# Kernel tuning notes

Measured on AMD Instinct MI355X. Metric: run time of the kernel, lower is better.

Reference implementation:

```python
import jax, jax.numpy as jnp
import numpy as np

EPS = 1e-5
NB, NP, NA, NROT = 16, 1024, 12, 60
C0, C1 = 64, 128
CIN, CFEAT, COUT = 256, 512, 256


def _bn(x, g, b):
    # training-mode BatchNorm1d: stats over batch (+ spatial) dims, channel dim 1
    axes = (0,) if x.ndim == 2 else (0, 2)
    m = x.mean(axis=axes, keepdims=True)
    v = x.var(axis=axes, keepdims=True)
    sh = [1] * x.ndim; sh[1] = -1
    return (x - m) * jax.lax.rsqrt(v + EPS) * g.reshape(sh) + b.reshape(sh)


def _hat(v):  # (n,3) -> (n,3,3) skew-symmetric
    z = jnp.zeros_like(v[:, 0])
    return jnp.stack([z, -v[:, 2], v[:, 1],
                      v[:, 2], z, -v[:, 0],
                      -v[:, 1], v[:, 0], z], axis=-1).reshape(-1, 3, 3)


def _exp_so3(v):  # Rodrigues formula, (n,3) -> (n,3,3)
    theta = jnp.linalg.norm(v, axis=-1, keepdims=True)  # (n,1)
    k = v / jnp.where(theta < 1e-8, 1.0, theta)
    K = _hat(k)
    s = jnp.sin(theta)[..., None]
    c = (1.0 - jnp.cos(theta))[..., None]
    I = jnp.eye(3, dtype=v.dtype)
    return I + s * K + c * (K @ K)


def _pointnet(xyz, feats, W, b, g, bb):
    # PointnetSO3Conv: concat xyz (expanded over anchors) with feats, 1x1 conv, max over points
    nb, _, npts, na = feats.shape
    x = jnp.concatenate([jnp.broadcast_to(xyz[:, :, :, None], (nb, 3, npts, na)), feats], axis=1)
    y = jnp.einsum('oc,bcpa->bopa', W, x) + b[None, :, None, None]
    y = y.max(axis=2)  # max over points -> (nb, o, na)
    return jax.nn.relu(_bn(y, g, bb))


def setup_inputs() -> dict:
    key = jax.random.key(0)
    ks = iter(jax.random.split(key, 64))
    def nrm(shape, s=0.1):
        return jax.random.normal(next(ks), shape, dtype=jnp.float32) * s
    d = {
        'xyz0': nrm((NB, 3, NP), 1.0),
        'feats0': nrm((NB, C0, NP, NA), 1.0),
        'xyz1': nrm((NB, 3, NP), 1.0),
        'feats1': nrm((NB, C1, NP, NA), 1.0),
        'trace_idx': jax.random.randint(next(ks), (NA, NROT), 0, NA),
        'anchors': nrm((NROT, 3, 3), 1.0),
        'pn0_W': nrm((C0, C0 + 3)), 'pn0_b': nrm((C0,)), 'pn0_g': jnp.ones((C0,), jnp.float32), 'pn0_bb': jnp.zeros((C0,), jnp.float32),
        'pn1_W': nrm((C1, C1 + 3)), 'pn1_b': nrm((C1,)), 'pn1_g': jnp.ones((C1,), jnp.float32), 'pn1_bb': jnp.zeros((C1,), jnp.float32),
        'lin_W': nrm((CIN, C0 + C1)), 'lin_b': nrm((CIN,)), 'lin_g': jnp.ones((CIN,), jnp.float32), 'lin_bb': jnp.zeros((CIN,), jnp.float32),
        'feat_W': nrm((CFEAT, CIN * NA)), 'feat_b': nrm((CFEAT,)), 'feat_g': jnp.ones((CFEAT,), jnp.float32), 'feat_bb': jnp.zeros((CFEAT,), jnp.float32),
        'att_W1': nrm((128, CFEAT)), 'att_b1': nrm((128,)), 'att_g': jnp.ones((128,), jnp.float32), 'att_bb': jnp.zeros((128,), jnp.float32),
        'att_W2': nrm((1, 128)), 'att_b2': nrm((1,)),
        'reg_W1': nrm((128, CFEAT)), 'reg_b1': nrm((128,)), 'reg_g': jnp.ones((128,), jnp.float32), 'reg_bb': jnp.zeros((128,), jnp.float32),
        'reg_W2': nrm((7, 128)), 'reg_b2': nrm((7,)),
        'out_W1': nrm((CFEAT, CFEAT)), 'out_b1': nrm((CFEAT,)), 'out_g': jnp.ones((CFEAT,), jnp.float32), 'out_bb': jnp.zeros((CFEAT,), jnp.float32),
        'out_W2': nrm((COUT, CFEAT)), 'out_b2': nrm((COUT,)),
    }
    return d


def reference(xyz0, feats0, xyz1, feats1, trace_idx, anchors,
              pn0_W, pn0_b, pn0_g, pn0_bb, pn1_W, pn1_b, pn1_g, pn1_bb,
              lin_W, lin_b, lin_g, lin_bb, feat_W, feat_b, feat_g, feat_bb,
              att_W1, att_b1, att_g, att_bb, att_W2, att_b2,
              reg_W1, reg_b1, reg_g, reg_bb, reg_W2, reg_b2,
              out_W1, out_b1, out_g, out_bb, out_W2, out_b2):
    nb = feats0.shape[0]
    # _pooling: per-level pointnet + BN + relu, concat, pn_linear + pn_bn
    p0 = _pointnet(xyz0, feats0, pn0_W, pn0_b, pn0_g, pn0_bb)
    p1 = _pointnet(xyz1, feats1, pn1_W, pn1_b, pn1_g, pn1_bb)
    x = jnp.concatenate([p0, p1], axis=1)                                   # (nb, 192, na)
    x = _bn(jnp.einsum('oc,bca->boa', lin_W, x) + lin_b[None, :, None], lin_g, lin_bb)  # (nb,256,na)
    # gather trace_idx_ori and flatten channel x anchor dims
    x = x[:, :, trace_idx].reshape(nb, CIN * NA, NROT)                      # (nb,3072,60)
    xf = jax.nn.relu(_bn(jnp.einsum('oc,bca->boa', feat_W, x) + feat_b[None, :, None], feat_g, feat_bb))  # (nb,512,60)
    h = jax.nn.relu(_bn(jnp.einsum('oc,bca->boa', reg_W1, xf) + reg_b1[None, :, None], reg_g, reg_bb))
    residual = (jnp.einsum('oc,bca->boa', reg_W2, h) + reg_b2[None, :, None]).transpose(0, 2, 1)  # (nb,60,7)
    res_D = residual[:, :, :3] / jnp.linalg.norm(residual[:, :, :3], axis=-1, keepdims=True)
    res_N = (jax.nn.sigmoid(residual[:, :, 3]) - 0.5) * jnp.pi / 5
    res_V = res_D * res_N[..., None]
    res_R = _exp_so3(res_V.reshape(-1, 3)).reshape(nb, NROT, 3, 3)
    res_T = residual[:, :, 4:]
    pred_R = jnp.einsum('tij,btjk->btik', anchors, res_R)
    # attention head + softmax over 60 rotations
    a = jax.nn.relu(_bn(jnp.einsum('oc,bca->boa', att_W1, xf) + att_b1[None, :, None], att_g, att_bb))
    logits = (jnp.einsum('oc,bca->boa', att_W2, a) + att_b2[None, :, None])[:, 0]   # (nb,60)
    x_attn = jax.nn.softmax(logits, axis=-1)
    # max-pool over rotations + out MLP
    xm = xf.max(axis=-1)                                                    # (nb,512)
    o = jax.nn.relu(_bn(xm @ out_W1.T + out_b1, out_g, out_bb))
    x_out = o @ out_W2.T + out_b2
    return (x_out, x_attn, pred_R, res_T)
```

## Files before the change

kernel.cpp:

```cpp
#include <hip/hip_runtime.h>
#include <math.h>

#define NBATCH 16
#define NPTS   1024
#define NANG   12
#define NROTS  60
#define EPSV   1e-5f

#define WB0_OFF   0
#define WB1_OFF   3072
#define PART0_OFF 13312
#define PART1_OFF 799744
#define XF_OFF    13312
#define XM_OFF    504832
#define OACT_OFF  513024
#define XCAT_OFF  2372608
#define XLIN_OFF  2409472
#define XG_OFF    2458624
#define BRP_OFF   2458624
#define HACT_OFF  4424704
#define AACT_OFF  4547584
#define FRAW_OFF  5407744
#define FEATW_OFF 6882304
#define XP0_OFF   8455168
#define XP1_OFF   14746624

#define OUT_XOUT 0
#define OUT_ATTN 4096
#define OUT_PRED 5056
#define OUT_REST 13696

typedef short  bf16x8 __attribute__((ext_vector_type(8)));
typedef float  f32x4  __attribute__((ext_vector_type(4)));

__device__ __forceinline__ unsigned short f2bf_rne(float x){
  unsigned int u = __float_as_uint(x);
  u += 0x7FFFu + ((u >> 16) & 1u);
  return (unsigned short)(u >> 16);
}
__device__ __forceinline__ float bf2f(unsigned short h){
  return __uint_as_float(((unsigned int)h) << 16);
}

__device__ __forceinline__ bf16x8 pack8(const float* f){
  union { unsigned int u[4]; bf16x8 v; } r;
  #pragma unroll
  for (int i = 0; i < 4; i++)
    r.u[i] = __builtin_amdgcn_perm(__float_as_uint(f[2*i+1]),
                                   __float_as_uint(f[2*i]), 0x07060302u);
  return r.v;
}

__device__ __forceinline__ void stage16(const unsigned short* g, unsigned short* l){
  __builtin_amdgcn_global_load_lds((const __attribute__((address_space(1))) void*)g,
                                   (__attribute__((address_space(3))) void*)l, 16, 0, 0);
}

template<int NT>
__device__ __forceinline__ void block_stats(float v, float& m, float& var, float* sbuf){
  constexpr int NW = NT / 64;
  float s = v, s2 = v * v;
  #pragma unroll
  for (int off = 32; off; off >>= 1){
    s  += __shfl_xor(s,  off, 64);
    s2 += __shfl_xor(s2, off, 64);
  }
  const int w = threadIdx.x >> 6;
  if ((threadIdx.x & 63) == 0){ sbuf[w] = s; sbuf[NW + w] = s2; }
  __syncthreads();
  float ts = 0.f, ts2 = 0.f;
  #pragma unroll
  for (int i = 0; i < NW; i++){ ts += sbuf[i]; ts2 += sbuf[NW + i]; }
  m = ts / (float)NT;
  var = ts2 / (float)NT - m * m;
}

#define TB0 6248
#define TB1 7784
template<int C>
__device__ __forceinline__ void prep_wb_body(int idx, const float* __restrict__ W,
                                             unsigned short* __restrict__ Wb){
  constexpr int KPAD = C + 32;
  if (idx >= C * KPAD) return;
  const int o = idx / KPAD, k = idx % KPAD;
  float v = 0.f;
  if (k < C)          v = W[(size_t)o * (C + 3) + 3 + k];
  else if (k < C + 3) v = W[(size_t)o * (C + 3) + (k - C)];
  Wb[idx] = f2bf_rne(v);
}

__global__ __launch_bounds__(256) void prep_all(
    const float* __restrict__ W0, const float* __restrict__ W1,
    const float* __restrict__ FW,
    const float* __restrict__ feats0, const float* __restrict__ feats1,
    unsigned short* __restrict__ wb0, unsigned short* __restrict__ wb1,
    unsigned short* __restrict__ fw2,
    unsigned short* __restrict__ xp0, unsigned short* __restrict__ xp1){
  __shared__ unsigned short tr[32][258];
  const int blk = blockIdx.x;
  if (blk < 24){
    prep_wb_body<64>(blk * 256 + threadIdx.x, W0, wb0);
    return;
  }
  if (blk < 104){
    prep_wb_body<128>((blk - 24) * 256 + threadIdx.x, W1, wb1);
    return;
  }
  if (blk < TB0){
    const int idx = (blk - 104) * 256 + threadIdx.x;
    const int o = idx / 3072, k = idx % 3072;
    const float x = FW[idx];
    const unsigned short hi = f2bf_rne(x);
    const unsigned short lo = f2bf_rne(x - bf2f(hi));
    fw2[(size_t)o * 6144 + k] = hi;
    fw2[(size_t)o * 6144 + 3072 + k] = lo;
    return;
  }
  const float* src; unsigned short* dst;
  if (blk < TB1){
    const int tb = blk - TB0;
    const int nt = tb % 48, kt = tb / 48;
    src = feats0 + (size_t)kt * 32 * 12288 + nt * 256;
    dst = xp0 + ((size_t)kt * 12288 + nt * 256) * 32;
  } else {
    const int tb = blk - TB1;
    const int nt = tb % 48, kt = tb / 48;
    src = feats1 + (size_t)kt * 32 * 12288 + nt * 256;
    dst = xp1 + ((size_t)kt * 12288 + nt * 256) * 32;
  }
  const int t = threadIdx.x;
  #pragma unroll
  for (int q = 0; q < 8; q++){
    const int idx = q * 256 + t;
    const int rr = idx >> 6, c4 = (idx & 63) << 2;
    const float4 v = *(const float4*)(src + (size_t)rr * 12288 + c4);
    tr[rr][c4 + 0] = (unsigned short)(__float_as_uint(v.x) >> 16);
    tr[rr][c4 + 1] = (unsigned short)(__float_as_uint(v.y) >> 16);
    tr[rr][c4 + 2] = (unsigned short)(__float_as_uint(v.z) >> 16);
    tr[rr][c4 + 3] = (unsigned short)(__float_as_uint(v.w) >> 16);
  }
  __syncthreads();
  union { unsigned short s[32]; bf16x8 v8[4]; } ob;
  #pragma unroll
  for (int j = 0; j < 32; j++) ob.s[j] = tr[j][t];
  unsigned short* dp = dst + (size_t)t * 32;
  #pragma unroll
  for (int q = 0; q < 4; q++)
    *(bf16x8*)(dp + q * 8) = ob.v8[q];
}

#define SROW 196
template<int C>
__device__ __forceinline__ void pn_body(
    int nchunk, int b,
    const float* __restrict__ xyz, const unsigned short* __restrict__ Xp,
    const unsigned short* __restrict__ Wb, float* __restrict__ part,
    float* yb ){
  constexpr int KPAD = C + 32;
  constexpr int NFK  = C / 32;
  constexpr int MTH  = C / 32;
  const int tid  = threadIdx.x;
  const int lane = tid & 63, w = tid >> 6;
  const int wo = w >> 2, wn = w & 3;
  const int g = lane >> 4, l16 = lane & 15;
  const int o_off = wo * (C / 2);
  const int nbase = nchunk * 192;

  int nn[3], pp[3];
  #pragma unroll
  for (int t = 0; t < 3; t++){
    nn[t] = wn * 48 + t * 16 + l16;
    pp[t] = (nbase + nn[t]) / 12;
  }

  f32x4 acc[MTH][3];
  #pragma unroll
  for (int m = 0; m < MTH; m++)
    #pragma unroll
    for (int t = 0; t < 3; t++)
      acc[m][t] = (f32x4){0.f, 0.f, 0.f, 0.f};

  const unsigned short* xbase = Xp + (size_t)b * NFK * 12288 * 32 + g * 8;
  bf16x8 Bf[NFK][3];
  #pragma unroll
  for (int ks = 0; ks < NFK; ks++)
    #pragma unroll
    for (int t = 0; t < 3; t++)
      Bf[ks][t] = *(const bf16x8*)(xbase + ((size_t)ks * 12288 + nbase + nn[t]) * 32);

  #pragma unroll
  for (int ks = 0; ks < NFK; ks++){
    const int kb = ks * 32;
    #pragma unroll
    for (int m = 0; m < MTH; m++){
      const bf16x8 Af = *(const bf16x8*)(Wb + (size_t)(o_off + m * 16 + l16) * KPAD + kb + g * 8);
      #pragma unroll
      for (int t = 0; t < 3; t++)
        acc[m][t] = __builtin_amdgcn_mfma_f32_16x16x32_bf16(Af, Bf[ks][t], acc[m][t], 0, 0, 0);
    }
  }

  {
    const int kb = C;
    bf16x8 Bf2[3];
    #pragma unroll
    for (int t = 0; t < 3; t++){
      float f[8];
      #pragma unroll
      for (int j = 0; j < 8; j++) f[j] = 0.f;
      if (g == 0){
        #pragma unroll
        for (int j = 0; j < 3; j++)
          f[j] = xyz[(size_t)(b * 3 + j) * NPTS + pp[t]];
      }
      Bf2[t] = pack8(f);
    }
    #pragma unroll
    for (int m = 0; m < MTH; m++){
      const bf16x8 Af = *(const bf16x8*)(Wb + (size_t)(o_off + m * 16 + l16) * KPAD + kb + g * 8);
      #pragma unroll
      for (int t = 0; t < 3; t++)
        acc[m][t] = __builtin_amdgcn_mfma_f32_16x16x32_bf16(Af, Bf2[t], acc[m][t], 0, 0, 0);
    }
  }

  float* myb = yb + wo * (16 * SROW);
  #pragma unroll
  for (int m = 0; m < MTH; m++){
    __syncthreads();
    #pragma unroll
    for (int t = 0; t < 3; t++)
      #pragma unroll
      for (int r = 0; r < 4; r++)
        myb[(g * 4 + r) * SROW + nn[t]] = acc[m][t][r];
    __syncthreads();
    const int lt = tid & 255;
    if (lt < 192){
      const int o_l = lt / 12, a = lt % 12;
      float mx = -3.4e38f;
      #pragma unroll
      for (int pl = 0; pl < 16; pl++)
        mx = fmaxf(mx, myb[o_l * SROW + pl * 12 + a]);
      part[((size_t)(b * 64 + nchunk) * C + o_off + m * 16 + o_l) * 12 + a] = mx;
    }
  }
}

__global__ __launch_bounds__(512, 4) void pn_both(
    const float* __restrict__ xyz0, const unsigned short* __restrict__ xp0,
    const unsigned short* __restrict__ wb0, float* __restrict__ part0,
    const float* __restrict__ xyz1, const unsigned short* __restrict__ xp1,
    const unsigned short* __restrict__ wb1, float* __restrict__ part1){
  __shared__ float yb[2 * 16 * SROW];
  const int lin   = blockIdx.x + 64 * (blockIdx.y + 16 * blockIdx.z);
  const int which = lin & 1;
  const int rest  = lin >> 1;
  const int nchunk = rest & 63, b = rest >> 6;
  if (which == 0) pn_body<64> (nchunk, b, xyz0, xp0, wb0, part0, yb);
  else            pn_body<128>(nchunk, b, xyz1, xp1, wb1, part1, yb);
}

__global__ void pn_reduce_bn(const float* __restrict__ part0, const float* __restrict__ part1,
    const float* __restrict__ b0, const float* __restrict__ g0, const float* __restrict__ bb0,
    const float* __restrict__ b1, const float* __restrict__ g1, const float* __restrict__ bb1,
    float* __restrict__ xcat){
  const int ch = blockIdx.x, t = threadIdx.x;
  const int b = t / 12, a = t % 12;
  const float* part; const float *bias, *g, *bb; int o, Cl;
  if (ch < 64){ part = part0; bias = b0; g = g0; bb = bb0; o = ch;      Cl = 64;  }
  else        { part = part1; bias = b1; g = g1; bb = bb1; o = ch - 64; Cl = 128; }
  const float* pp = part + ((size_t)(b * 64) * Cl + o) * 12 + a;
  const size_t kstride = (size_t)Cl * 12;
  float v = pp[0];
  for (int k = 1; k < 64; k++) v = fmaxf(v, pp[(size_t)k * kstride]);
  v += bias[o];
  __shared__ float sbuf[8];
  float m, var;
  block_stats<192>(v, m, var, sbuf);
  float xn = (v - m) * rsqrtf(var + EPSV) * g[o] + bb[o];
  xcat[((size_t)b * 192 + ch) * 12 + a] = fmaxf(xn, 0.f);
}

__global__ void lin_bn(const float* __restrict__ xcat, const float* __restrict__ W,
    const float* __restrict__ bias, const float* __restrict__ g, const float* __restrict__ bb,
    float* __restrict__ xlin){
  const int o = blockIdx.x, t = threadIdx.x;
  const int b = t / 12, a = t % 12;
  const float* xr = xcat + (size_t)b * 2304 + a;
  const float* wr = W + (size_t)o * 192;
  float v = bias[o];
  for (int c = 0; c < 192; c++) v = fmaf(wr[c], xr[(size_t)c * 12], v);
  __shared__ float sbuf[8];
  float m, var;
  block_stats<192>(v, m, var, sbuf);
  xlin[((size_t)b * 256 + o) * 12 + a] = (v - m) * rsqrtf(var + EPSV) * g[o] + bb[o];
}

__global__ void prep_xg(const float* __restrict__ xlin, const int* __restrict__ trace,
                        unsigned short* __restrict__ Xg){
  const int n = blockIdx.x;
  const int b = n / 60, r = n % 60;
  unsigned short* row = Xg + (size_t)n * 6144;
  __shared__ int ta[12];
  if (threadIdx.x < 12) ta[threadIdx.x] = trace[threadIdx.x * 60 + r];
  __syncthreads();
  for (int i = threadIdx.x; i < 3072; i += 256){
    const int c = i / 12, a = i % 12;
    const float x = xlin[((size_t)b * 256 + c) * 12 + ta[a]];
    const unsigned short hi = f2bf_rne(x);
    const unsigned short lo = f2bf_rne(x - bf2f(hi));
    row[i] = hi;
    row[3072 + i] = lo;
  }
}

__global__ __launch_bounds__(256) void feat_mfma(
    const unsigned short* __restrict__ Wb2, const unsigned short* __restrict__ Xg,
    float* __restrict__ fraw){
  const int nblk = blockIdx.x, mblk = blockIdx.y, seg = blockIdx.z;
  const int tid = threadIdx.x;
  const int lane = tid & 63, wave = tid >> 6;
  const int g = lane >> 4, l16 = lane & 15;
  const int kA = (seg == 1) ? 3072 : 0;
  const int kB = (seg == 2) ? 3072 : 0;
  const int sw = l16 & 7;
  const int wm = wave >> 1, wn = wave & 1;

  __shared__ unsigned short As[2][64 * 64];
  __shared__ unsigned short Bs[2][64 * 64];

  int rowj[2], colj[2], ldsoff[2];
  #pragma unroll
  for (int j = 0; j < 2; j++){
    const int idx = j * 256 + wave * 64 + lane;
    rowj[j]   = idx >> 3;
    colj[j]   = ((idx & 7) ^ (rowj[j] & 7)) * 8;
    ldsoff[j] = (j * 256 + wave * 64) * 8;
  }
  const unsigned short* Agb = Wb2 + (size_t)mblk * 64 * 6144 + kA;
  const unsigned short* Bgb = Xg  + (size_t)nblk * 64 * 6144 + kB;

  f32x4 acc[2][2];
  #pragma unroll
  for (int i = 0; i < 2; i++)
    #pragma unroll
    for (int j = 0; j < 2; j++)
      acc[i][j] = (f32x4){0.f, 0.f, 0.f, 0.f};

  #pragma unroll
  for (int j = 0; j < 2; j++){
    stage16(Agb + (size_t)rowj[j] * 6144 + colj[j], &As[0][ldsoff[j]]);
    stage16(Bgb + (size_t)rowj[j] * 6144 + colj[j], &Bs[0][ldsoff[j]]);
  }
  __syncthreads();

  for (int kc = 0; kc < 3072; kc += 64){
    const int buf = (kc >> 6) & 1;
    if (kc + 64 < 3072){
      const int kn = kc + 64;
      #pragma unroll
      for (int j = 0; j < 2; j++){
        stage16(Agb + (size_t)rowj[j] * 6144 + kn + colj[j], &As[buf ^ 1][ldsoff[j]]);
        stage16(Bgb + (size_t)rowj[j] * 6144 + kn + colj[j], &Bs[buf ^ 1][ldsoff[j]]);
      }
    }
    #pragma unroll
    for (int kc2 = 0; kc2 < 64; kc2 += 32){
      const int c0 = kc2 >> 3;
      bf16x8 af[2], bfr[2];
      #pragma unroll
      for (int i = 0; i < 2; i++)
        af[i]  = *(const bf16x8*)&As[buf][(wm * 32 + i * 16 + l16) * 64 + ((c0 + g) ^ sw) * 8];
      #pragma unroll
      for (int i = 0; i < 2; i++)
        bfr[i] = *(const bf16x8*)&Bs[buf][(wn * 32 + i * 16 + l16) * 64 + ((c0 + g) ^ sw) * 8];
      #pragma unroll
      for (int i = 0; i < 2; i++)
        #pragma unroll
        for (int j = 0; j < 2; j++)
          acc[i][j] = __builtin_amdgcn_mfma_f32_16x16x32_bf16(af[i], bfr[j], acc[i][j], 0, 0, 0);
    }
    __syncthreads();
  }

  float* base = fraw + (size_t)seg * (512 * 960);
  #pragma unroll
  for (int i = 0; i < 2; i++)
    #pragma unroll
    for (int j = 0; j < 2; j++){
      const int n = nblk * 64 + wn * 32 + j * 16 + l16;
      #pragma unroll
      for (int q = 0; q < 4; q++){
        const int m = mblk * 64 + wm * 32 + i * 16 + g * 4 + q;
        base[(size_t)m * 960 + n] = acc[i][j][q];
      }
    }
}

__global__ void feat_bn(const float* __restrict__ fraw, const float* __restrict__ bias,
    const float* __restrict__ g, const float* __restrict__ bb,
    float* __restrict__ xf, float* __restrict__ xm){
  const int o = blockIdx.x, t = threadIdx.x;
  const int b = t / 60, r = t % 60;
  const size_t SS = (size_t)512 * 960;
  const size_t in = (size_t)o * 960 + t;
  float v = fraw[in] + fraw[SS + in] + fraw[2 * SS + in] + bias[o];
  __shared__ float sbuf[32];
  float m, var;
  block_stats<960>(v, m, var, sbuf);
  const float xn = fmaxf((v - m) * rsqrtf(var + EPSV) * g[o] + bb[o], 0.f);
  xf[((size_t)b * 512 + o) * 60 + r] = xn;
  __shared__ float red[960];
  red[t] = xn;
  __syncthreads();
  if (r == 0){
    float mx = red[t];
    for (int k = 1; k < 60; k++) mx = fmaxf(mx, red[t + k]);
    xm[(size_t)b * 512 + o] = mx;
  }
}

__global__ __launch_bounds__(256) void brgemm_oh1(const float* __restrict__ xf,
    const float* __restrict__ Wr, const float* __restrict__ Wa,
    float* __restrict__ brp,
    const float* __restrict__ xm, const float* __restrict__ oW1,
    const float* __restrict__ ob1, const float* __restrict__ og,
    const float* __restrict__ obb, float* __restrict__ o_act){
  const int z = blockIdx.z;
  if (z == 16){
    const int q = blockIdx.y * 4 + blockIdx.x;
    if (q >= 32) return;
    const int t = threadIdx.x;
    const int b = t & 15, j = t >> 4;
    const int oc = q * 16 + j;
    float acc = ob1[oc];
    const float* wr = oW1 + (size_t)oc * 512;
    const float* xr = xm + (size_t)b * 512;
    for (int c = 0; c < 512; c++) acc = fmaf(wr[c], xr[c], acc);
    float s = acc, s2 = acc * acc;
    #pragma unroll
    for (int off = 8; off; off >>= 1){
      s  += __shfl_xor(s,  off, 16);
      s2 += __shfl_xor(s2, off, 16);
    }
    const float m = s * (1.f / 16.f);
    const float var = s2 * (1.f / 16.f) - m * m;
    o_act[(size_t)b * 512 + oc] = fmaxf((acc - m) * rsqrtf(var + EPSV) * og[oc] + obb[oc], 0.f);
    return;
  }
  const int og_ = blockIdx.x, b = blockIdx.y;
  const int br = z >> 3, ks = z & 7;
  const float* W = br ? Wa : Wr;
  const int lane = threadIdx.x & 63, wave = threadIdx.x >> 6;
  const int obase = og_ * 32 + wave * 8;
  const int rr = lane < 60 ? lane : 0;
  const float* xb = xf + ((size_t)b * 512 + ks * 64) * 60 + rr;
  const float* wr = W + (size_t)obase * 512 + ks * 64;

  float acc[8];
  #pragma unroll
  for (int i = 0; i < 8; i++) acc[i] = 0.f;

  float cur[4], nxt[4];
  #pragma unroll
  for (int j = 0; j < 4; j++) cur[j] = xb[(size_t)j * 60];

  for (int c0 = 0; c0 < 64; c0 += 4){
    #pragma unroll
    for (int j = 0; j < 4; j++){
      int cc = c0 + 4 + j; if (cc > 63) cc = 63;
      nxt[j] = xb[(size_t)cc * 60];
    }
    #pragma unroll
    for (int j = 0; j < 4; j++)
      #pragma unroll
      for (int i = 0; i < 8; i++)
        acc[i] = fmaf(wr[(size_t)i * 512 + c0 + j], cur[j], acc[i]);
    #pragma unroll
    for (int j = 0; j < 4; j++) cur[j] = nxt[j];
  }

  if (lane < 60){
    #pragma unroll
    for (int i = 0; i < 8; i++)
      brp[(((size_t)z * NBATCH + b) * 128 + obase + i) * 60 + lane] = acc[i];
  }
}

__global__ void br_bn(const float* __restrict__ brp,
    const float* __restrict__ biasR, const float* __restrict__ gR, const float* __restrict__ bbR,
    const float* __restrict__ biasA, const float* __restrict__ gA, const float* __restrict__ bbA,
    float* __restrict__ hact, float* __restrict__ aact){
  const int o = blockIdx.x, br = blockIdx.y, t = threadIdx.x;
  const int b = t / 60, r = t % 60;
  const float* bias = br ? biasA : biasR;
  const float* g    = br ? gA    : gR;
  const float* bb   = br ? bbA   : bbR;
  float v = bias[o];
  #pragma unroll
  for (int ks = 0; ks < 8; ks++)
    v += brp[((((size_t)br * 8 + ks) * NBATCH + b) * 128 + o) * 60 + r];
  __shared__ float sbuf[32];
  float m, var;
  block_stats<960>(v, m, var, sbuf);
  float* outp = br ? aact : hact;
  outp[((size_t)b * 128 + o) * 60 + r] =
      fmaxf((v - m) * rsqrtf(var + EPSV) * g[o] + bb[o], 0.f);
}

__global__ void heads(
    const float* __restrict__ h, const float* __restrict__ rW2,
    const float* __restrict__ rb2, const float* __restrict__ anchors,
    const float* __restrict__ a, const float* __restrict__ aW2, const float* __restrict__ ab2,
    const float* __restrict__ o_act, const float* __restrict__ oW2,
    const float* __restrict__ ob2, float* __restrict__ out){
  const int b = blockIdx.x, sel = blockIdx.y, t = threadIdx.x;
  if (sel == 0){
    if (t >= 64) return;
    const int r = t < 60 ? t : 59;
    float res[7];
    #pragma unroll
    for (int j = 0; j < 7; j++) res[j] = rb2[j];
    for (int c = 0; c < 128; c++){
      const float hv = h[((size_t)b * 128 + c) * 60 + r];
      #pragma unroll
      for (int j = 0; j < 7; j++) res[j] = fmaf(rW2[j * 128 + c], hv, res[j]);
    }
    if (t >= 60) return;
    const float n = sqrtf(res[0]*res[0] + res[1]*res[1] + res[2]*res[2]);
    const float invn = 1.f / n;
    const float Nv = (1.f / (1.f + expf(-res[3])) - 0.5f) * 3.14159265358979323846f / 5.f;
    const float v0 = res[0]*invn*Nv, v1 = res[1]*invn*Nv, v2 = res[2]*invn*Nv;
    const float th = sqrtf(v0*v0 + v1*v1 + v2*v2);
    const float invt = th < 1e-8f ? 1.f : 1.f / th;
    const float k0 = v0*invt, k1 = v1*invt, k2 = v2*invt;
    const float s = sinf(th), cc = 1.f - cosf(th);
    const float K[9] = {0.f, -k2, k1,  k2, 0.f, -k0,  -k1, k0, 0.f};
    float K2[9];
    #pragma unroll
    for (int ii = 0; ii < 3; ii++)
      #pragma unroll
      for (int jj = 0; jj < 3; jj++)
        K2[ii*3+jj] = K[ii*3+0]*K[0*3+jj] + K[ii*3+1]*K[1*3+jj] + K[ii*3+2]*K[2*3+jj];
    float R[9];
    #pragma unroll
    for (int ii = 0; ii < 3; ii++)
      #pragma unroll
      for (int jj = 0; jj < 3; jj++)
        R[ii*3+jj] = (ii == jj ? 1.f : 0.f) + s * K[ii*3+jj] + cc * K2[ii*3+jj];
    const float* A = anchors + (size_t)t * 9;
    #pragma unroll
    for (int ii = 0; ii < 3; ii++)
      #pragma unroll
      for (int kk = 0; kk < 3; kk++){
        const float pv = A[ii*3+0]*R[0*3+kk] + A[ii*3+1]*R[1*3+kk] + A[ii*3+2]*R[2*3+kk];
        out[OUT_PRED + ((size_t)b * 60 + t) * 9 + ii * 3 + kk] = pv;
      }
    #pragma unroll
    for (int k = 0; k < 3; k++)
      out[OUT_REST + ((size_t)b * 60 + t) * 3 + k] = res[4 + k];
  } else if (sel == 1){
    if (t >= 64) return;
    const int r = t < 60 ? t : 59;
    float acc = ab2[0];
    for (int c = 0; c < 128; c++)
      acc = fmaf(aW2[c], a[((size_t)b * 128 + c) * 60 + r], acc);
    const float l = t < 60 ? acc : -INFINITY;
    float mx = l;
    #pragma unroll
    for (int off = 32; off; off >>= 1) mx = fmaxf(mx, __shfl_xor(mx, off, 64));
    const float e = t < 60 ? expf(l - mx) : 0.f;
    float ssum = e;
    #pragma unroll
    for (int off = 32; off; off >>= 1) ssum += __shfl_xor(ssum, off, 64);
    if (t < 60) out[OUT_ATTN + (size_t)b * 60 + t] = e / ssum;
  } else {
    const float* wr = oW2 + (size_t)t * 512;
    const float* xr = o_act + (size_t)b * 512;
    float acc = ob2[t];
    for (int c = 0; c < 512; c++) acc = fmaf(wr[c], xr[c], acc);
    out[OUT_XOUT + (size_t)b * 256 + t] = acc;
  }
}

extern "C" void kernel_launch(void* const* d_in, const int* in_sizes, int n_in,
                              void* d_out, int out_size, void* d_ws, size_t ws_size,
                              hipStream_t stream){
  const float* xyz0    = (const float*)d_in[0];
  const float* feats0  = (const float*)d_in[1];
  const float* xyz1    = (const float*)d_in[2];
  const float* feats1  = (const float*)d_in[3];
  const int*   trace   = (const int*)  d_in[4];
  const float* anchors = (const float*)d_in[5];
  const float* pn0_W  = (const float*)d_in[6];
  const float* pn0_b  = (const float*)d_in[7];
  const float* pn0_g  = (const float*)d_in[8];
  const float* pn0_bb = (const float*)d_in[9];
  const float* pn1_W  = (const float*)d_in[10];
  const float* pn1_b  = (const float*)d_in[11];
  const float* pn1_g  = (const float*)d_in[12];
  const float* pn1_bb = (const float*)d_in[13];
  const float* lin_W  = (const float*)d_in[14];
  const float* lin_b  = (const float*)d_in[15];
  const float* lin_g  = (const float*)d_in[16];
  const float* lin_bb = (const float*)d_in[17];
  const float* feat_W  = (const float*)d_in[18];
  const float* feat_b  = (const float*)d_in[19];
  const float* feat_g  = (const float*)d_in[20];
  const float* feat_bb = (const float*)d_in[21];
  const float* att_W1 = (const float*)d_in[22];
  const float* att_b1 = (const float*)d_in[23];
  const float* att_g  = (const float*)d_in[24];
  const float* att_bb = (const float*)d_in[25];
  const float* att_W2 = (const float*)d_in[26];
  const float* att_b2 = (const float*)d_in[27];
  const float* reg_W1 = (const float*)d_in[28];
  const float* reg_b1 = (const float*)d_in[29];
  const float* reg_g  = (const float*)d_in[30];
  const float* reg_bb = (const float*)d_in[31];
  const float* reg_W2 = (const float*)d_in[32];
  const float* reg_b2 = (const float*)d_in[33];
  const float* out_W1 = (const float*)d_in[34];
  const float* out_b1 = (const float*)d_in[35];
  const float* out_g  = (const float*)d_in[36];
  const float* out_bb = (const float*)d_in[37];
  const float* out_W2 = (const float*)d_in[38];
  const float* out_b2 = (const float*)d_in[39];

  float* ws  = (float*)d_ws;
  float* out = (float*)d_out;
  unsigned short* wb0 = (unsigned short*)(ws + WB0_OFF);
  unsigned short* wb1 = (unsigned short*)(ws + WB1_OFF);
  unsigned short* fw  = (unsigned short*)(ws + FEATW_OFF);
  unsigned short* xg  = (unsigned short*)(ws + XG_OFF);
  unsigned short* xp0 = (unsigned short*)(ws + XP0_OFF);
  unsigned short* xp1 = (unsigned short*)(ws + XP1_OFF);

  prep_all<<<10856, 256, 0, stream>>>(pn0_W, pn1_W, feat_W, feats0, feats1,
                                      wb0, wb1, fw, xp0, xp1);

  pn_both<<<dim3(64, 16, 2), 512, 0, stream>>>(xyz0, xp0, wb0, ws + PART0_OFF,
                                               xyz1, xp1, wb1, ws + PART1_OFF);

  pn_reduce_bn<<<192, 192, 0, stream>>>(ws + PART0_OFF, ws + PART1_OFF,
      pn0_b, pn0_g, pn0_bb, pn1_b, pn1_g, pn1_bb, ws + XCAT_OFF);

  lin_bn<<<256, 192, 0, stream>>>(ws + XCAT_OFF, lin_W, lin_b, lin_g, lin_bb, ws + XLIN_OFF);

  prep_xg<<<960, 256, 0, stream>>>(ws + XLIN_OFF, trace, xg);

  feat_mfma<<<dim3(15, 8, 3), 256, 0, stream>>>(fw, xg, ws + FRAW_OFF);

  feat_bn<<<512, 960, 0, stream>>>(ws + FRAW_OFF, feat_b, feat_g, feat_bb,
                                   ws + XF_OFF, ws + XM_OFF);

  brgemm_oh1<<<dim3(4, 16, 17), 256, 0, stream>>>(ws + XF_OFF, reg_W1, att_W1, ws + BRP_OFF,
      ws + XM_OFF, out_W1, out_b1, out_g, out_bb, ws + OACT_OFF);

  br_bn<<<dim3(128, 2), 960, 0, stream>>>(ws + BRP_OFF,
      reg_b1, reg_g, reg_bb, att_b1, att_g, att_bb,
      ws + HACT_OFF, ws + AACT_OFF);

  heads<<<dim3(16, 3), 256, 0, stream>>>(ws + HACT_OFF, reg_W2, reg_b2, anchors,
      ws + AACT_OFF, att_W2, att_b2, ws + OACT_OFF, out_W2, out_b2, out);
}
```

Baseline: 466.1 us.

## Split prep and pointnet launches to overlap feats1 transpose with pn0 compute

Prep of the weights and the feats0 transpose now run in their own kernel. A second kernel runs the feats1 transpose, the pn0 pointnet GEMM and the split of the feat weights into hi/lo bf16 together, and pn1 gets a separate launch. The goal is to overlap the memory-bound transpose of the larger feats1 tensor with the compute of pn0. The transpose store is also reworked to use 8-element vector stores spread across more threads. The cost is one extra launch, plus a mixed kernel whose shared-memory and register limits are set by the pn body.

```diff
diff --git a/kernel.cpp b/kernel.cpp
--- a/kernel.cpp
+++ b/kernel.cpp
@@ -75,8 +75,33 @@
   var = ts2 / (float)NT - m * m;
 }
 
-#define TB0 6248
-#define TB1 7784
+template<int NT>
+__device__ __forceinline__ void transpose_tile(const float* __restrict__ src,
+    unsigned short* __restrict__ dst, unsigned short (*tr)[258], int t){
+  constexpr int QL = 2048 / NT;
+  #pragma unroll
+  for (int q = 0; q < QL; q++){
+    const int idx = q * NT + t;
+    const int rr = idx >> 6, c4 = (idx & 63) << 2;
+    const float4 v = *(const float4*)(src + (size_t)rr * 12288 + c4);
+    tr[rr][c4 + 0] = (unsigned short)(__float_as_uint(v.x) >> 16);
+    tr[rr][c4 + 1] = (unsigned short)(__float_as_uint(v.y) >> 16);
+    tr[rr][c4 + 2] = (unsigned short)(__float_as_uint(v.z) >> 16);
+    tr[rr][c4 + 3] = (unsigned short)(__float_as_uint(v.w) >> 16);
+  }
+  __syncthreads();
+  constexpr int QS = 1024 / NT;
+  #pragma unroll
+  for (int p = 0; p < QS; p++){
+    const int gl = p * NT + t;
+    const int col = gl >> 2, kq = gl & 3;
+    union { unsigned short s[8]; bf16x8 v; } ob;
+    #pragma unroll
+    for (int j = 0; j < 8; j++) ob.s[j] = tr[kq * 8 + j][col];
+    *(bf16x8*)(dst + (size_t)col * 32 + kq * 8) = ob.v;
+  }
+}
+
 template<int C>
 __device__ __forceinline__ void prep_wb_body(int idx, const float* __restrict__ W,
                                              unsigned short* __restrict__ Wb){
@@ -89,64 +114,22 @@
   Wb[idx] = f2bf_rne(v);
 }
 
-__global__ __launch_bounds__(256) void prep_all(
+__global__ __launch_bounds__(256) void prep_a(
+    const float* __restrict__ feats0, unsigned short* __restrict__ xp0,
     const float* __restrict__ W0, const float* __restrict__ W1,
-    const float* __restrict__ FW,
-    const float* __restrict__ feats0, const float* __restrict__ feats1,
-    unsigned short* __restrict__ wb0, unsigned short* __restrict__ wb1,
-    unsigned short* __restrict__ fw2,
-    unsigned short* __restrict__ xp0, unsigned short* __restrict__ xp1){
+    unsigned short* __restrict__ wb0, unsigned short* __restrict__ wb1){
   __shared__ unsigned short tr[32][258];
   const int blk = blockIdx.x;
-  if (blk < 24){
-    prep_wb_body<64>(blk * 256 + threadIdx.x, W0, wb0);
-    return;
-  }
-  if (blk < 104){
-    prep_wb_body<128>((blk - 24) * 256 + threadIdx.x, W1, wb1);
-    return;
-  }
-  if (blk < TB0){
-    const int idx = (blk - 104) * 256 + threadIdx.x;
-    const int o = idx / 3072, k = idx % 3072;
-    const float x = FW[idx];
-    const unsigned short hi = f2bf_rne(x);
-    const unsigned short lo = f2bf_rne(x - bf2f(hi));
-    fw2[(size_t)o * 6144 + k] = hi;
-    fw2[(size_t)o * 6144 + 3072 + k] = lo;
-    return;
-  }
-  const float* src; unsigned short* dst;
-  if (blk < TB1){
-    const int tb = blk - TB0;
-    const int nt = tb % 48, kt = tb / 48;
-    src = feats0 + (size_t)kt * 32 * 12288 + nt * 256;
-    dst = xp0 + ((size_t)kt * 12288 + nt * 256) * 32;
+  if (blk < 1536){
+    const int nt = blk % 48, kt = blk / 48;
+    transpose_tile<256>(feats0 + (size_t)kt * 32 * 12288 + nt * 256,
+                        xp0 + ((size_t)kt * 12288 + nt * 256) * 32,
+                        tr, threadIdx.x);
+  } else if (blk < 1560){
+    prep_wb_body<64>((blk - 1536) * 256 + threadIdx.x, W0, wb0);
   } else {
-    const int tb = blk - TB1;
-    const int nt = tb % 48, kt = tb / 48;
-    src = feats1 + (size_t)kt * 32 * 12288 + nt * 256;
-    dst = xp1 + ((size_t)kt * 12288 + nt * 256) * 32;
-  }
-  const int t = threadIdx.x;
-  #pragma unroll
-  for (int q = 0; q < 8; q++){
-    const int idx = q * 256 + t;
-    const int rr = idx >> 6, c4 = (idx & 63) << 2;
-    const float4 v = *(const float4*)(src + (size_t)rr * 12288 + c4);
-    tr[rr][c4 + 0] = (unsigned short)(__float_as_uint(v.x) >> 16);
-    tr[rr][c4 + 1] = (unsigned short)(__float_as_uint(v.y) >> 16);
-    tr[rr][c4 + 2] = (unsigned short)(__float_as_uint(v.z) >> 16);
-    tr[rr][c4 + 3] = (unsigned short)(__float_as_uint(v.w) >> 16);
-  }
-  __syncthreads();
-  union { unsigned short s[32]; bf16x8 v8[4]; } ob;
-  #pragma unroll
-  for (int j = 0; j < 32; j++) ob.s[j] = tr[j][t];
-  unsigned short* dp = dst + (size_t)t * 32;
-  #pragma unroll
-  for (int q = 0; q < 4; q++)
-    *(bf16x8*)(dp + q * 8) = ob.v8[q];
+    prep_wb_body<128>((blk - 1560) * 256 + threadIdx.x, W1, wb1);
+  }
 }
 
 #define SROW 196
@@ -246,18 +229,37 @@
   }
 }
 
-__global__ __launch_bounds__(512, 4) void pn_both(
+__global__ __launch_bounds__(512, 4) void prep_b(
+    const float* __restrict__ feats1, unsigned short* __restrict__ xp1,
     const float* __restrict__ xyz0, const unsigned short* __restrict__ xp0,
     const unsigned short* __restrict__ wb0, float* __restrict__ part0,
+    const float* __restrict__ FW, unsigned short* __restrict__ fw2){
+  __shared__ float smem[2 * 16 * SROW];
+  const int blk = blockIdx.x;
+  if (blk < 3072){
+    const int nt = blk % 48, kt = blk / 48;
+    transpose_tile<512>(feats1 + (size_t)kt * 32 * 12288 + nt * 256,
+                        xp1 + ((size_t)kt * 12288 + nt * 256) * 32,
+                        (unsigned short (*)[258])smem, threadIdx.x);
+  } else if (blk < 4096){
+    const int blk2 = blk - 3072;
+    pn_body<64>(blk2 & 63, blk2 >> 6, xyz0, xp0, wb0, part0, smem);
+  } else {
+    const int idx = (blk - 4096) * 512 + threadIdx.x;
+    const int o = idx / 3072, k = idx % 3072;
+    const float x = FW[idx];
+    const unsigned short hi = f2bf_rne(x);
+    const unsigned short lo = f2bf_rne(x - bf2f(hi));
+    fw2[(size_t)o * 6144 + k] = hi;
+    fw2[(size_t)o * 6144 + 3072 + k] = lo;
+  }
+}
+
+__global__ __launch_bounds__(512, 4) void pn1(
     const float* __restrict__ xyz1, const unsigned short* __restrict__ xp1,
     const unsigned short* __restrict__ wb1, float* __restrict__ part1){
   __shared__ float yb[2 * 16 * SROW];
-  const int lin   = blockIdx.x + 64 * (blockIdx.y + 16 * blockIdx.z);
-  const int which = lin & 1;
-  const int rest  = lin >> 1;
-  const int nchunk = rest & 63, b = rest >> 6;
-  if (which == 0) pn_body<64> (nchunk, b, xyz0, xp0, wb0, part0, yb);
-  else            pn_body<128>(nchunk, b, xyz1, xp1, wb1, part1, yb);
+  pn_body<128>(blockIdx.x, blockIdx.y, xyz1, xp1, wb1, part1, yb);
 }
 
 __global__ void pn_reduce_bn(const float* __restrict__ part0, const float* __restrict__ part1,
@@ -636,11 +638,11 @@
   unsigned short* xp0 = (unsigned short*)(ws + XP0_OFF);
   unsigned short* xp1 = (unsigned short*)(ws + XP1_OFF);
 
-  prep_all<<<10856, 256, 0, stream>>>(pn0_W, pn1_W, feat_W, feats0, feats1,
-                                      wb0, wb1, fw, xp0, xp1);
-
-  pn_both<<<dim3(64, 16, 2), 512, 0, stream>>>(xyz0, xp0, wb0, ws + PART0_OFF,
-                                               xyz1, xp1, wb1, ws + PART1_OFF);
+  prep_a<<<1640, 256, 0, stream>>>(feats0, xp0, pn0_W, pn1_W, wb0, wb1);
+
+  prep_b<<<7168, 512, 0, stream>>>(feats1, xp1, xyz0, xp0, wb0, ws + PART0_OFF, feat_W, fw);
+
+  pn1<<<dim3(64, 16), 512, 0, stream>>>(xyz1, xp1, wb1, ws + PART1_OFF);
 
   pn_reduce_bn<<<192, 192, 0, stream>>>(ws + PART0_OFF, ws + PART1_OFF,
       pn0_b, pn0_g, pn0_bb, pn1_b, pn1_g, pn1_bb, ws + XCAT_OFF);
```

New measurement: 441.2 us. 5.3% less time.
